# Optimization experiments

Hardware: AMD Instinct MI355X
Metric: run time of the kernel (lower is better)

## Reference

```python
import jax, jax.numpy as jnp
import numpy as np

HIDDEN = 2048
NUM_Q_HEADS = 32
NUM_KV_HEADS = 8
HEAD_DIM = HIDDEN // NUM_Q_HEADS          # 64
GROUP = NUM_Q_HEADS // NUM_KV_HEADS       # 4
B, L = 2, 2048


def setup_inputs() -> dict:
    key = jax.random.key(0)
    ks = jax.random.split(key, 10)
    s = 1.0 / np.sqrt(HIDDEN)
    return {
        "x": jax.random.normal(ks[0], (B, L, HIDDEN), dtype=jnp.float32),
        "attention_mask": jnp.ones((B, L), dtype=jnp.int32),
        "q_w": jax.random.uniform(ks[1], (NUM_Q_HEADS * HEAD_DIM, HIDDEN), jnp.float32, -s, s),
        "q_b": jax.random.uniform(ks[2], (NUM_Q_HEADS * HEAD_DIM,), jnp.float32, -s, s),
        "k_w": jax.random.uniform(ks[3], (NUM_KV_HEADS * HEAD_DIM, HIDDEN), jnp.float32, -s, s),
        "k_b": jax.random.uniform(ks[4], (NUM_KV_HEADS * HEAD_DIM,), jnp.float32, -s, s),
        "v_w": jax.random.uniform(ks[5], (NUM_KV_HEADS * HEAD_DIM, HIDDEN), jnp.float32, -s, s),
        "v_b": jax.random.uniform(ks[6], (NUM_KV_HEADS * HEAD_DIM,), jnp.float32, -s, s),
        "o_w": jax.random.uniform(ks[7], (HIDDEN, HIDDEN), jnp.float32, -s, s),
        "o_b": jax.random.uniform(ks[8], (HIDDEN,), jnp.float32, -s, s),
    }


def reference(x, attention_mask, q_w, q_b, k_w, k_b, v_w, v_b, o_w, o_b):
    Bsz, Ls, _ = x.shape
    # projections (torch Linear: x @ W^T + b)
    q = x @ q_w.T + q_b                      # [B, L, Hq*D]
    k = x @ k_w.T + k_b                      # [B, L, Hkv*D]
    v = x @ v_w.T + v_b                      # [B, L, Hkv*D]
    # grouped reshape: q head h = kv*GROUP + g, matching repeat_interleave on k/v
    q = q.reshape(Bsz, Ls, NUM_KV_HEADS, GROUP, HEAD_DIM)
    k = k.reshape(Bsz, Ls, NUM_KV_HEADS, HEAD_DIM)
    v = v.reshape(Bsz, Ls, NUM_KV_HEADS, HEAD_DIM)
    scale = 1.0 / np.sqrt(HEAD_DIM).astype(np.float32)
    # scores: [B, Hkv, G, Lq, Lk]
    scores = jnp.einsum('bqhgd,bkhd->bhgqk', q, k) * scale
    neg = jnp.finfo(scores.dtype).min
    # causal mask
    causal = jnp.triu(jnp.ones((Ls, Ls), dtype=bool), k=1)
    scores = jnp.where(causal, neg, scores)
    # key padding mask: attention_mask==0 -> masked
    pad = (attention_mask == 0)[:, None, None, None, :]  # [B,1,1,1,Lk]
    scores = jnp.where(pad, neg, scores)
    attn = jax.nn.softmax(scores, axis=-1)
    # dropout is identity in eval / p=0
    out = jnp.einsum('bhgqk,bkhd->bqhgd', attn, v)
    out = out.reshape(Bsz, Ls, HIDDEN)
    return out @ o_w.T + o_b
```

## Files before the change

kernel.cpp:

```cpp
#include <hip/hip_runtime.h>
#include <hip/hip_bf16.h>

typedef __attribute__((ext_vector_type(8))) short s16x8;
typedef __attribute__((ext_vector_type(4))) short s16x4;
typedef __attribute__((ext_vector_type(2))) short s16x2;
typedef __attribute__((ext_vector_type(4))) float f32x4;
typedef __attribute__((ext_vector_type(4))) unsigned int u32x4;

#define L_ 2048
#define HID 2048
#define DH 64

__device__ __forceinline__ short f2bs(float f) {
    __hip_bfloat16 h = __float2bfloat16(f);
    return *reinterpret_cast<short*>(&h);
}
__device__ __forceinline__ unsigned int pkbf_fast(float a, float b) {
    unsigned ua = __builtin_bit_cast(unsigned, a) + 0x8000u;
    unsigned ub = __builtin_bit_cast(unsigned, b) + 0x8000u;
    return __builtin_amdgcn_perm(ub, ua, 0x07060302u);
}
__device__ __forceinline__ float bpermf(int byteidx, float v) {
    int r = __builtin_amdgcn_ds_bpermute(byteidx, __builtin_bit_cast(int, v));
    return __builtin_bit_cast(float, r);
}
__device__ __forceinline__ s16x4 load4_bf16(const float* p) {
    const float4 v = *(const float4*)p;
    s16x4 r; r.x = f2bs(v.x); r.y = f2bs(v.y); r.z = f2bs(v.z); r.w = f2bs(v.w);
    return r;
}
__device__ __forceinline__ s16x4 load4_bf16(const __hip_bfloat16* p) {
    return *(const s16x4*)p;
}
__device__ __forceinline__ void store1(float* p, float v) { *p = v; }
__device__ __forceinline__ void store1(__hip_bfloat16* p, float v) { *p = __float2bfloat16(v); }

__device__ __forceinline__ void glds16(const __hip_bfloat16* g, __hip_bfloat16* l) {
    __builtin_amdgcn_global_load_lds(
        (const __attribute__((address_space(1))) unsigned int*)g,
        (__attribute__((address_space(3))) unsigned int*)l, 16, 0, 0);
}

__device__ __forceinline__ void cvt8_body(const float* src, __hip_bfloat16* dst, long i) {
    const float4* p = (const float4*)src + i * 2;
    const float4 a = p[0], b = p[1];
    s16x8 r;
    r[0] = f2bs(a.x); r[1] = f2bs(a.y); r[2] = f2bs(a.z); r[3] = f2bs(a.w);
    r[4] = f2bs(b.x); r[5] = f2bs(b.y); r[6] = f2bs(b.z); r[7] = f2bs(b.w);
    *((s16x8*)dst + i) = r;
}

__global__ __launch_bounds__(256) void cvt_xqkv(
    const float* __restrict__ x,  const float* __restrict__ qw,
    const float* __restrict__ kw, const float* __restrict__ vw,
    __hip_bfloat16* __restrict__ xb,  __hip_bfloat16* __restrict__ qwb,
    __hip_bfloat16* __restrict__ kwb, __hip_bfloat16* __restrict__ vwb)
{
    long i = (long)blockIdx.x * 256 + threadIdx.x;
    const float* src; __hip_bfloat16* dst;
    if (i < 1048576)      { src = x;  dst = xb;  }
    else if (i < 1572864) { src = qw; dst = qwb; i -= 1048576; }
    else if (i < 1703936) { src = kw; dst = kwb; i -= 1572864; }
    else                  { src = vw; dst = vwb; i -= 1703936; }
    cvt8_body(src, dst, i);
}

__global__ __launch_bounds__(256) void cvt8(const float* __restrict__ in,
                                            __hip_bfloat16* __restrict__ out, int n8) {
    const int i = blockIdx.x * 256 + threadIdx.x;
    if (i >= n8) return;
    cvt8_body(in, out, i);
}

__global__ __launch_bounds__(256) void gemm_qkv(
    const __hip_bfloat16* __restrict__ A,
    const __hip_bfloat16* __restrict__ W,
    const float* __restrict__ qb, const float* __restrict__ kb2,
    const float* __restrict__ vb2,
    __hip_bfloat16* __restrict__ Qb, __hip_bfloat16* __restrict__ Kt,
    __hip_bfloat16* __restrict__ Vt)
{
    const int K = 2048;
    __shared__ __hip_bfloat16 sA[128*32];
    __shared__ __hip_bfloat16 sB[128*32];
    const int tid  = threadIdx.x;
    const int wid  = tid >> 6;
    const int lane = tid & 63;
    const int m0 = blockIdx.x * 128;
    const int n0 = blockIdx.y * 128;
    const int wm = (wid >> 1) * 64;
    const int wn = (wid & 1) * 64;

    f32x4 acc[4][4];
#pragma unroll
    for (int i = 0; i < 4; ++i)
#pragma unroll
        for (int j = 0; j < 4; ++j)
#pragma unroll
            for (int r = 0; r < 4; ++r) acc[i][j][r] = 0.0f;

    const int sr = tid >> 2;
    const int sc = (tid & 3) * 8;
    const __hip_bfloat16* gA = A + (long)(m0 + sr) * K + sc;
    const __hip_bfloat16* gB = W + (long)(n0 + sr) * K + sc;
    __hip_bfloat16* lA = &sA[sr*32 + sc];
    __hip_bfloat16* lB = &sB[sr*32 + sc];

    const int arow0 = wm + (lane & 15);
    const int brow0 = wn + (lane & 15);
    const int koff  = (lane >> 4) * 8;

    for (int kt = 0; kt < 64; ++kt) {
        glds16(gA,              lA);
        glds16(gA + (long)64*K, lA + 64*32);
        glds16(gB,              lB);
        glds16(gB + (long)64*K, lB + 64*32);
        gA += 32; gB += 32;
        __syncthreads();

        s16x8 af[4], bfr[4];
#pragma unroll
        for (int mi = 0; mi < 4; ++mi)
            af[mi] = *(const s16x8*)&sA[(arow0 + mi*16)*32 + koff];
#pragma unroll
        for (int ni = 0; ni < 4; ++ni)
            bfr[ni] = *(const s16x8*)&sB[(brow0 + ni*16)*32 + koff];
#pragma unroll
        for (int mi = 0; mi < 4; ++mi)
#pragma unroll
            for (int ni = 0; ni < 4; ++ni)
                acc[mi][ni] = __builtin_amdgcn_mfma_f32_16x16x32_bf16(
                    af[mi], bfr[ni], acc[mi][ni], 0, 0, 0);
        __syncthreads();
    }

    __hip_bfloat16* C; int ldc, coff; const float* bias;
    if (n0 < 2048)      { C = Qb; ldc = 2048; coff = n0;        bias = qb  + n0; }
    else if (n0 < 2560) { C = Kt; ldc = 512;  coff = n0 - 2048; bias = kb2 + (n0 - 2048); }
    else                { C = Vt; ldc = 512;  coff = n0 - 2560; bias = vb2 + (n0 - 2560); }

    float bvals[4];
#pragma unroll
    for (int ni = 0; ni < 4; ++ni)
        bvals[ni] = bias[wn + ni*16 + (lane & 15)];
#pragma unroll
    for (int mi = 0; mi < 4; ++mi) {
        const int row = m0 + wm + mi*16 + (lane >> 4)*4;
#pragma unroll
        for (int ni = 0; ni < 4; ++ni) {
            const int col = coff + wn + ni*16 + (lane & 15);
#pragma unroll
            for (int r = 0; r < 4; ++r)
                C[(long)(row + r)*ldc + col] = __float2bfloat16(acc[mi][ni][r] + bvals[ni]);
        }
    }
}

template <typename TC>
__global__ __launch_bounds__(256) void gemm_fast(
    const __hip_bfloat16* __restrict__ A,
    const __hip_bfloat16* __restrict__ Bw,
    const float* __restrict__ bias,
    TC* __restrict__ C, int M, int N, int K)
{
    __shared__ __hip_bfloat16 sA[128*32];
    __shared__ __hip_bfloat16 sB[128*32];
    const int tid  = threadIdx.x;
    const int wid  = tid >> 6;
    const int lane = tid & 63;
    const int m0 = blockIdx.x * 128;
    const int n0 = blockIdx.y * 128;
    const int wm = (wid >> 1) * 64;
    const int wn = (wid & 1) * 64;

    f32x4 acc[4][4];
#pragma unroll
    for (int i = 0; i < 4; ++i)
#pragma unroll
        for (int j = 0; j < 4; ++j)
#pragma unroll
            for (int r = 0; r < 4; ++r) acc[i][j][r] = 0.0f;

    const int sr = tid >> 2;
    const int sc = (tid & 3) * 8;
    const __hip_bfloat16* gA = A  + (long)(m0 + sr) * K + sc;
    const __hip_bfloat16* gB = Bw + (long)(n0 + sr) * K + sc;
    __hip_bfloat16* lA = &sA[sr*32 + sc];
    __hip_bfloat16* lB = &sB[sr*32 + sc];

    const int arow0 = wm + (lane & 15);
    const int brow0 = wn + (lane & 15);
    const int koff  = (lane >> 4) * 8;

    const int nk = K >> 5;
    for (int kt = 0; kt < nk; ++kt) {
        glds16(gA,              lA);
        glds16(gA + (long)64*K, lA + 64*32);
        glds16(gB,              lB);
        glds16(gB + (long)64*K, lB + 64*32);
        gA += 32; gB += 32;
        __syncthreads();

        s16x8 af[4], bfr[4];
#pragma unroll
        for (int mi = 0; mi < 4; ++mi)
            af[mi] = *(const s16x8*)&sA[(arow0 + mi*16)*32 + koff];
#pragma unroll
        for (int ni = 0; ni < 4; ++ni)
            bfr[ni] = *(const s16x8*)&sB[(brow0 + ni*16)*32 + koff];
#pragma unroll
        for (int mi = 0; mi < 4; ++mi)
#pragma unroll
            for (int ni = 0; ni < 4; ++ni)
                acc[mi][ni] = __builtin_amdgcn_mfma_f32_16x16x32_bf16(
                    af[mi], bfr[ni], acc[mi][ni], 0, 0, 0);
        __syncthreads();
    }

    float bvals[4];
#pragma unroll
    for (int ni = 0; ni < 4; ++ni)
        bvals[ni] = bias[n0 + wn + ni*16 + (lane & 15)];
#pragma unroll
    for (int mi = 0; mi < 4; ++mi) {
        const int row = m0 + wm + mi*16 + (lane >> 4)*4;
#pragma unroll
        for (int ni = 0; ni < 4; ++ni) {
            const int col = n0 + wn + ni*16 + (lane & 15);
#pragma unroll
            for (int r = 0; r < 4; ++r)
                store1(&C[(long)(row + r)*N + col], acc[mi][ni][r] + bvals[ni]);
        }
    }
}

template <typename TA, typename TC>
__global__ __launch_bounds__(256) void gemm_bt_bias(
    const TA* __restrict__ A, const float* __restrict__ Bw,
    const float* __restrict__ bias, TC* __restrict__ C,
    int M, int N, int K)
{
    __shared__ __hip_bfloat16 sA[128*32];
    __shared__ __hip_bfloat16 sB[128*32];
    const int tid  = threadIdx.x;
    const int wid  = tid >> 6;
    const int lane = tid & 63;
    const int m0 = blockIdx.x * 128;
    const int n0 = blockIdx.y * 128;
    const int wm = (wid >> 1) * 64;
    const int wn = (wid & 1) * 64;

    f32x4 acc[4][4];
#pragma unroll
    for (int i = 0; i < 4; ++i)
#pragma unroll
        for (int j = 0; j < 4; ++j)
#pragma unroll
            for (int r = 0; r < 4; ++r) acc[i][j][r] = 0.0f;

    const int sr = tid >> 3;
    const int sc = (tid & 7) * 4;
    const TA*    gA = A  + (long)(m0 + sr) * K + sc;
    const float* gB = Bw + (long)(n0 + sr) * K + sc;

    const int arow0 = wm + (lane & 15);
    const int brow0 = wn + (lane & 15);
    const int koff  = (lane >> 4) * 8;

    const int nk = K >> 5;
    for (int kt = 0; kt < nk; ++kt) {
        s16x4 a0 = load4_bf16(gA);
        s16x4 a1 = load4_bf16(gA + (long)32*K);
        s16x4 a2 = load4_bf16(gA + (long)64*K);
        s16x4 a3 = load4_bf16(gA + (long)96*K);
        s16x4 b0 = load4_bf16(gB);
        s16x4 b1 = load4_bf16(gB + (long)32*K);
        s16x4 b2 = load4_bf16(gB + (long)64*K);
        s16x4 b3 = load4_bf16(gB + (long)96*K);
        gA += 32; gB += 32;
        *(s16x4*)&sA[(sr     )*32 + sc] = a0;
        *(s16x4*)&sA[(sr + 32)*32 + sc] = a1;
        *(s16x4*)&sA[(sr + 64)*32 + sc] = a2;
        *(s16x4*)&sA[(sr + 96)*32 + sc] = a3;
        *(s16x4*)&sB[(sr     )*32 + sc] = b0;
        *(s16x4*)&sB[(sr + 32)*32 + sc] = b1;
        *(s16x4*)&sB[(sr + 64)*32 + sc] = b2;
        *(s16x4*)&sB[(sr + 96)*32 + sc] = b3;
        __syncthreads();

        s16x8 af[4], bfr[4];
#pragma unroll
        for (int mi = 0; mi < 4; ++mi)
            af[mi] = *(const s16x8*)&sA[(arow0 + mi*16)*32 + koff];
#pragma unroll
        for (int ni = 0; ni < 4; ++ni)
            bfr[ni] = *(const s16x8*)&sB[(brow0 + ni*16)*32 + koff];
#pragma unroll
        for (int mi = 0; mi < 4; ++mi)
#pragma unroll
            for (int ni = 0; ni < 4; ++ni)
                acc[mi][ni] = __builtin_amdgcn_mfma_f32_16x16x32_bf16(
                    af[mi], bfr[ni], acc[mi][ni], 0, 0, 0);
        __syncthreads();
    }

    float bvals[4];
#pragma unroll
    for (int ni = 0; ni < 4; ++ni)
        bvals[ni] = bias[n0 + wn + ni*16 + (lane & 15)];
#pragma unroll
    for (int mi = 0; mi < 4; ++mi) {
        const int row = m0 + wm + mi*16 + (lane >> 4)*4;
#pragma unroll
        for (int ni = 0; ni < 4; ++ni) {
            const int col = n0 + wn + ni*16 + (lane & 15);
#pragma unroll
            for (int r = 0; r < 4; ++r)
                store1(&C[(long)(row + r)*N + col], acc[mi][ni][r] + bvals[ni]);
        }
    }
}

#define LDK 72
#define LDV 72

__global__ __launch_bounds__(512, 6) void gqa_flash(
    const __hip_bfloat16* __restrict__ Q,
    const __hip_bfloat16* __restrict__ Kb,
    const __hip_bfloat16* __restrict__ Vb,
    const int* __restrict__ amask,
    __hip_bfloat16* __restrict__ O)
{
    __shared__ __hip_bfloat16 sK[2][64*LDK];
    __shared__ __hip_bfloat16 sVt[2][64*LDV];
    __shared__ unsigned int sPp[8][512];

    const int tid  = threadIdx.x;
    const int wid  = tid >> 6;
    const int lane = tid & 63;
    const int bx = blockIdx.x;
    const int bh = blockIdx.y;
    const int b  = bh >> 5;
    const int h  = bh & 31;
    const int kv = h >> 2;

    const __hip_bfloat16* Kg = Kb + (long)(b*L_)*512 + kv*DH;
    const __hip_bfloat16* Vg = Vb + (long)(b*L_)*512 + kv*DH;
    const int* mg = amask + b*L_;

    const int lcol = lane & 15;
    const int g    = lane >> 4;

    const int kr = tid >> 3;
    const int kc = (tid & 7) * 8;
    const int vj = (tid & 31) * 2;
    const int vd = (tid >> 5) * 4;
    const int qsr = tid >> 2;
    const int qsc = (tid & 3) * 16;

    unsigned int* myP = sPp[wid];
    const float c1 = 0.18033688011112042f;

    for (int ph = 0; ph < 2; ++ph) {
        const int qt = ph ? (15 - bx) : bx;
        const int jmax = 2*qt + 1;
        const __hip_bfloat16* Qg = Q + (long)(b*L_ + qt*128)*HID + h*DH;

        __syncthreads();
        {
            s16x8 q0 = *(const s16x8*)(Qg + (long)qsr*HID + qsc);
            s16x8 q1 = *(const s16x8*)(Qg + (long)qsr*HID + qsc + 8);
            __hip_bfloat16* dst = (qsr < 64) ? &sK[0][qsr*LDK + qsc]
                                             : &sK[1][(qsr-64)*LDK + qsc];
            *(s16x8*)&dst[0] = q0;
            *(s16x8*)&dst[8] = q1;
        }
        __syncthreads();
        s16x8 qf[2];
        {
            const __hip_bfloat16* qbuf = (wid < 4)
                ? &sK[0][((wid & 3)*16 + lcol)*LDK]
                : &sK[1][((wid & 3)*16 + lcol)*LDK];
            qf[0] = *(const s16x8*)&qbuf[g*8];
            qf[1] = *(const s16x8*)&qbuf[32 + g*8];
        }
        __syncthreads();

        {
            s16x8 k0 = *(const s16x8*)(Kg + (long)kr*512 + kc);
            *(s16x8*)&sK[0][kr*LDK + kc] = k0;
            s16x4 v0 = *(const s16x4*)(Vg + (long)vj*512 + vd);
            s16x4 v1 = *(const s16x4*)(Vg + (long)(vj+1)*512 + vd);
            short* sv = (short*)sVt[0];
#pragma unroll
            for (int i = 0; i < 4; ++i) {
                s16x2 pr; pr.x = v0[i]; pr.y = v1[i];
                *(s16x2*)&sv[(vd+i)*LDV + vj] = pr;
            }
        }

        float lrl = 0.0f;
        f32x4 oacc[4];
#pragma unroll
        for (int nt = 0; nt < 4; ++nt)
#pragma unroll
            for (int r = 0; r < 4; ++r) oacc[nt][r] = 0.0f;

        for (int jt = 0; jt <= jmax; ++jt) {
            const int cur = jt & 1;
            __syncthreads();

            const long pno = (long)((jt + 1)*64) * 512;
            s16x8 kreg = *(const s16x8*)(Kg + pno + (long)kr*512 + kc);
            s16x4 v0r  = *(const s16x4*)(Vg + pno + (long)vj*512 + vd);
            s16x4 v1r  = *(const s16x4*)(Vg + pno + (long)(vj+1)*512 + vd);
            const int mv = mg[jt*64 + lane];
            const unsigned long long bal = __ballot(mv == 0);

            f32x4 sacc[4];
#pragma unroll
            for (int ct = 0; ct < 4; ++ct)
#pragma unroll
                for (int r = 0; r < 4; ++r) sacc[ct][r] = 0.0f;
#pragma unroll
            for (int ks = 0; ks < 2; ++ks)
#pragma unroll
                for (int ct = 0; ct < 4; ++ct) {
                    s16x8 kf = *(const s16x8*)&sK[cur][(ct*16 + lcol)*LDK + ks*32 + g*8];
                    sacc[ct] = __builtin_amdgcn_mfma_f32_16x16x32_bf16(
                        kf, qf[ks], sacc[ct], 0, 0, 0);
                }

            if (bal) {
#pragma unroll
                for (int ct = 0; ct < 4; ++ct) {
                    const unsigned nib = (unsigned)(bal >> (ct*16 + g*4)) & 15u;
#pragma unroll
                    for (int r = 0; r < 4; ++r)
                        if (nib & (1u << r)) sacc[ct][r] = -2.0e5f;
                }
            }
            if (jt >= 2*qt) {
                const int qrow = qt*128 + wid*16 + lcol;
#pragma unroll
                for (int ct = 0; ct < 4; ++ct) {
                    const int jb = jt*64 + ct*16 + g*4;
#pragma unroll
                    for (int r = 0; r < 4; ++r)
                        if (jb + r > qrow) sacc[ct][r] = -2.0e5f;
                }
            }

            float ps = 0.0f;
#pragma unroll
            for (int ct = 0; ct < 4; ++ct) {
                const float p0 = exp2f(sacc[ct][0] * c1);
                const float p1 = exp2f(sacc[ct][1] * c1);
                const float p2 = exp2f(sacc[ct][2] * c1);
                const float p3 = exp2f(sacc[ct][3] * c1);
                ps += (p0 + p1) + (p2 + p3);
                const int xb = (ct & 1) << 4;
                myP[ct*128 +      ((g*16 + lcol) ^ xb)] = pkbf_fast(p0, p1);
                myP[ct*128 + 64 + ((g*16 + lcol) ^ xb)] = pkbf_fast(p2, p3);
            }
            lrl += ps;

            if (jt < jmax) {
                const int nb = cur ^ 1;
                *(s16x8*)&sK[nb][kr*LDK + kc] = kreg;
                short* sv = (short*)sVt[nb];
#pragma unroll
                for (int i = 0; i < 4; ++i) {
                    s16x2 pr; pr.x = v0r[i]; pr.y = v1r[i];
                    *(s16x2*)&sv[(vd+i)*LDV + vj] = pr;
                }
            }

#pragma unroll
            for (int ks = 0; ks < 2; ++ks) {
                const int ct = ks*2 + (g >> 1);
                const int xb = (ct & 1) << 4;
                const int w0 = (2*g) & 3;
                const int w1 = (2*g + 1) & 3;
                u32x4 pu;
                pu.x = myP[ct*128 +      ((w0*16 + lcol) ^ xb)];
                pu.y = myP[ct*128 + 64 + ((w0*16 + lcol) ^ xb)];
                pu.z = myP[ct*128 +      ((w1*16 + lcol) ^ xb)];
                pu.w = myP[ct*128 + 64 + ((w1*16 + lcol) ^ xb)];
                const s16x8 pf = __builtin_bit_cast(s16x8, pu);
#pragma unroll
                for (int nt = 0; nt < 4; ++nt) {
                    s16x8 vf = *(const s16x8*)&sVt[cur][(nt*16 + lcol)*LDV + ks*32 + g*8];
                    oacc[nt] = __builtin_amdgcn_mfma_f32_16x16x32_bf16(
                        pf, vf, oacc[nt], 0, 0, 0);
                }
            }
        }

        lrl += __shfl_xor(lrl, 16);
        lrl += __shfl_xor(lrl, 32);
        const float inv = 1.0f / lrl;
        float invr[4];
#pragma unroll
        for (int r = 0; r < 4; ++r)
            invr[r] = bpermf((g*4 + r) << 2, inv);

        __hip_bfloat16* Og = O + (long)(b*L_ + qt*128)*HID + h*DH;
#pragma unroll
        for (int r = 0; r < 4; ++r) {
            const int row = wid*16 + g*4 + r;
#pragma unroll
            for (int nt = 0; nt < 4; ++nt)
                Og[(long)row*HID + nt*16 + lcol] =
                    __float2bfloat16(oacc[nt][r] * invr[r]);
        }
    }
}

extern "C" void kernel_launch(void* const* d_in, const int* in_sizes, int n_in,
                              void* d_out, int out_size, void* d_ws, size_t ws_size,
                              hipStream_t stream) {
    const float* x   = (const float*)d_in[0];
    const int*   am  = (const int*)d_in[1];
    const float* q_w = (const float*)d_in[2];
    const float* q_b = (const float*)d_in[3];
    const float* k_w = (const float*)d_in[4];
    const float* k_b = (const float*)d_in[5];
    const float* v_w = (const float*)d_in[6];
    const float* v_b = (const float*)d_in[7];
    const float* o_w = (const float*)d_in[8];
    const float* o_b = (const float*)d_in[9];
    float* out = (float*)d_out;
    char* ws = (char*)d_ws;
    dim3 blk(256);

    if (ws_size >= 37748736) {
        __hip_bfloat16* Qb   = (__hip_bfloat16*)d_out;
        __hip_bfloat16* xb   = (__hip_bfloat16*)((char*)d_out + 16777216);
        __hip_bfloat16* wcat = (__hip_bfloat16*)(ws);
        __hip_bfloat16* qwb  = (__hip_bfloat16*)(ws);
        __hip_bfloat16* kwb  = (__hip_bfloat16*)(ws + 8388608);
        __hip_bfloat16* vwb  = (__hip_bfloat16*)(ws + 10485760);
        __hip_bfloat16* Kt   = (__hip_bfloat16*)(ws + 12582912);
        __hip_bfloat16* Vt   = (__hip_bfloat16*)(ws + 16777216);
        __hip_bfloat16* Ob   = (__hip_bfloat16*)(ws + 20971520);
        __hip_bfloat16* owb  = qwb;

        cvt_xqkv<<<7168, blk, 0, stream>>>(x, q_w, k_w, v_w, xb, qwb, kwb, vwb);
        gemm_qkv<<<dim3(32, 24), blk, 0, stream>>>(xb, wcat, q_b, k_b, v_b, Qb, Kt, Vt);
        cvt8<<<2048, blk, 0, stream>>>(o_w, owb, 524288);
        gqa_flash<<<dim3(8, 64), dim3(512), 0, stream>>>(Qb, Kt, Vt, am, Ob);
        gemm_fast<float><<<dim3(32, 16), blk, 0, stream>>>(Ob, owb, o_b, out, 4096, 2048, 2048);
    } else {
        __hip_bfloat16* Qb = (__hip_bfloat16*)d_out;
        __hip_bfloat16* Kt = (__hip_bfloat16*)(ws);
        __hip_bfloat16* Vt = (__hip_bfloat16*)(ws + 4194304);
        __hip_bfloat16* Ob = (__hip_bfloat16*)(ws + 8388608);
        gemm_bt_bias<float, __hip_bfloat16><<<dim3(32,16), blk, 0, stream>>>(x, q_w, q_b, Qb, 4096, 2048, 2048);
        gemm_bt_bias<float, __hip_bfloat16><<<dim3(32, 4), blk, 0, stream>>>(x, k_w, k_b, Kt, 4096,  512, 2048);
        gemm_bt_bias<float, __hip_bfloat16><<<dim3(32, 4), blk, 0, stream>>>(x, v_w, v_b, Vt, 4096,  512, 2048);
        gqa_flash<<<dim3(8, 64), dim3(512), 0, stream>>>(Qb, Kt, Vt, am, Ob);
        gemm_bt_bias<__hip_bfloat16, float><<<dim3(32,16), blk, 0, stream>>>(Ob, o_w, o_b, out, 4096, 2048, 2048);
    }
}
```

Before: 309.5 us.

## Fold softmax scale into Q projection and split paired q-tiles into separate blocks

The log2e/sqrt(d) softmax scale is applied in the QKV GEMM epilogue, so the attention inner loop no longer multiplies each score before exp2. The flash-attention kernel no longer handles two complementary q-tiles per block. It launches one q-tile per block with a doubled grid, ordered longest tiles first. This trades the built-in load balancing of the pairing for more blocks and better CU occupancy, and adds the Q reload and setup cost per block.

```diff
diff --git a/kernel.cpp b/kernel.cpp
--- a/kernel.cpp
+++ b/kernel.cpp
@@ -135,7 +135,9 @@
     }
 
     __hip_bfloat16* C; int ldc, coff; const float* bias;
-    if (n0 < 2048)      { C = Qb; ldc = 2048; coff = n0;        bias = qb  + n0; }
+    float csc = 1.0f;
+    if (n0 < 2048)      { C = Qb; ldc = 2048; coff = n0;        bias = qb  + n0;
+                          csc = 0.18033688011112042f; }
     else if (n0 < 2560) { C = Kt; ldc = 512;  coff = n0 - 2048; bias = kb2 + (n0 - 2048); }
     else                { C = Vt; ldc = 512;  coff = n0 - 2560; bias = vb2 + (n0 - 2560); }
 
@@ -151,7 +153,8 @@
             const int col = coff + wn + ni*16 + (lane & 15);
 #pragma unroll
             for (int r = 0; r < 4; ++r)
-                C[(long)(row + r)*ldc + col] = __float2bfloat16(acc[mi][ni][r] + bvals[ni]);
+                C[(long)(row + r)*ldc + col] =
+                    __float2bfloat16((acc[mi][ni][r] + bvals[ni]) * csc);
         }
     }
 }
@@ -238,7 +241,7 @@
 __global__ __launch_bounds__(256) void gemm_bt_bias(
     const TA* __restrict__ A, const float* __restrict__ Bw,
     const float* __restrict__ bias, TC* __restrict__ C,
-    int M, int N, int K)
+    int M, int N, int K, float scale)
 {
     __shared__ __hip_bfloat16 sA[128*32];
     __shared__ __hip_bfloat16 sB[128*32];
@@ -316,7 +319,8 @@
             const int col = n0 + wn + ni*16 + (lane & 15);
 #pragma unroll
             for (int r = 0; r < 4; ++r)
-                store1(&C[(long)(row + r)*N + col], acc[mi][ni][r] + bvals[ni]);
+                store1(&C[(long)(row + r)*N + col],
+                       (acc[mi][ni][r] + bvals[ni]) * scale);
         }
     }
 }
@@ -338,7 +342,7 @@
     const int tid  = threadIdx.x;
     const int wid  = tid >> 6;
     const int lane = tid & 63;
-    const int bx = blockIdx.x;
+    const int qt = 15 - blockIdx.x;
     const int bh = blockIdx.y;
     const int b  = bh >> 5;
     const int h  = bh & 31;
@@ -359,161 +363,156 @@
     const int qsc = (tid & 3) * 16;
 
     unsigned int* myP = sPp[wid];
-    const float c1 = 0.18033688011112042f;
-
-    for (int ph = 0; ph < 2; ++ph) {
-        const int qt = ph ? (15 - bx) : bx;
-        const int jmax = 2*qt + 1;
-        const __hip_bfloat16* Qg = Q + (long)(b*L_ + qt*128)*HID + h*DH;
-
-        __syncthreads();
-        {
-            s16x8 q0 = *(const s16x8*)(Qg + (long)qsr*HID + qsc);
-            s16x8 q1 = *(const s16x8*)(Qg + (long)qsr*HID + qsc + 8);
-            __hip_bfloat16* dst = (qsr < 64) ? &sK[0][qsr*LDK + qsc]
-                                             : &sK[1][(qsr-64)*LDK + qsc];
-            *(s16x8*)&dst[0] = q0;
-            *(s16x8*)&dst[8] = q1;
-        }
-        __syncthreads();
-        s16x8 qf[2];
-        {
-            const __hip_bfloat16* qbuf = (wid < 4)
-                ? &sK[0][((wid & 3)*16 + lcol)*LDK]
-                : &sK[1][((wid & 3)*16 + lcol)*LDK];
-            qf[0] = *(const s16x8*)&qbuf[g*8];
-            qf[1] = *(const s16x8*)&qbuf[32 + g*8];
-        }
-        __syncthreads();
-
-        {
-            s16x8 k0 = *(const s16x8*)(Kg + (long)kr*512 + kc);
-            *(s16x8*)&sK[0][kr*LDK + kc] = k0;
-            s16x4 v0 = *(const s16x4*)(Vg + (long)vj*512 + vd);
-            s16x4 v1 = *(const s16x4*)(Vg + (long)(vj+1)*512 + vd);
-            short* sv = (short*)sVt[0];
+
+    const int jmax = 2*qt + 1;
+    const __hip_bfloat16* Qg = Q + (long)(b*L_ + qt*128)*HID + h*DH;
+
+    {
+        s16x8 q0 = *(const s16x8*)(Qg + (long)qsr*HID + qsc);
+        s16x8 q1 = *(const s16x8*)(Qg + (long)qsr*HID + qsc + 8);
+        __hip_bfloat16* dst = (qsr < 64) ? &sK[0][qsr*LDK + qsc]
+                                         : &sK[1][(qsr-64)*LDK + qsc];
+        *(s16x8*)&dst[0] = q0;
+        *(s16x8*)&dst[8] = q1;
+    }
+    __syncthreads();
+    s16x8 qf[2];
+    {
+        const __hip_bfloat16* qbuf = (wid < 4)
+            ? &sK[0][((wid & 3)*16 + lcol)*LDK]
+            : &sK[1][((wid & 3)*16 + lcol)*LDK];
+        qf[0] = *(const s16x8*)&qbuf[g*8];
+        qf[1] = *(const s16x8*)&qbuf[32 + g*8];
+    }
+    __syncthreads();
+
+    {
+        s16x8 k0 = *(const s16x8*)(Kg + (long)kr*512 + kc);
+        *(s16x8*)&sK[0][kr*LDK + kc] = k0;
+        s16x4 v0 = *(const s16x4*)(Vg + (long)vj*512 + vd);
+        s16x4 v1 = *(const s16x4*)(Vg + (long)(vj+1)*512 + vd);
+        short* sv = (short*)sVt[0];
+#pragma unroll
+        for (int i = 0; i < 4; ++i) {
+            s16x2 pr; pr.x = v0[i]; pr.y = v1[i];
+            *(s16x2*)&sv[(vd+i)*LDV + vj] = pr;
+        }
+    }
+
+    float lrl = 0.0f;
+    f32x4 oacc[4];
+#pragma unroll
+    for (int nt = 0; nt < 4; ++nt)
+#pragma unroll
+        for (int r = 0; r < 4; ++r) oacc[nt][r] = 0.0f;
+
+    for (int jt = 0; jt <= jmax; ++jt) {
+        const int cur = jt & 1;
+        __syncthreads();
+
+        const long pno = (long)((jt + 1)*64) * 512;
+        s16x8 kreg = *(const s16x8*)(Kg + pno + (long)kr*512 + kc);
+        s16x4 v0r  = *(const s16x4*)(Vg + pno + (long)vj*512 + vd);
+        s16x4 v1r  = *(const s16x4*)(Vg + pno + (long)(vj+1)*512 + vd);
+        const int mv = mg[jt*64 + lane];
+        const unsigned long long bal = __ballot(mv == 0);
+
+        f32x4 sacc[4];
+#pragma unroll
+        for (int ct = 0; ct < 4; ++ct)
+#pragma unroll
+            for (int r = 0; r < 4; ++r) sacc[ct][r] = 0.0f;
+#pragma unroll
+        for (int ks = 0; ks < 2; ++ks)
+#pragma unroll
+            for (int ct = 0; ct < 4; ++ct) {
+                s16x8 kf = *(const s16x8*)&sK[cur][(ct*16 + lcol)*LDK + ks*32 + g*8];
+                sacc[ct] = __builtin_amdgcn_mfma_f32_16x16x32_bf16(
+                    kf, qf[ks], sacc[ct], 0, 0, 0);
+            }
+
+        if (bal) {
+#pragma unroll
+            for (int ct = 0; ct < 4; ++ct) {
+                const unsigned nib = (unsigned)(bal >> (ct*16 + g*4)) & 15u;
+#pragma unroll
+                for (int r = 0; r < 4; ++r)
+                    if (nib & (1u << r)) sacc[ct][r] = -2.0e5f;
+            }
+        }
+        if (jt >= 2*qt) {
+            const int qrow = qt*128 + wid*16 + lcol;
+#pragma unroll
+            for (int ct = 0; ct < 4; ++ct) {
+                const int jb = jt*64 + ct*16 + g*4;
+#pragma unroll
+                for (int r = 0; r < 4; ++r)
+                    if (jb + r > qrow) sacc[ct][r] = -2.0e5f;
+            }
+        }
+
+        float ps = 0.0f;
+#pragma unroll
+        for (int ct = 0; ct < 4; ++ct) {
+            const float p0 = exp2f(sacc[ct][0]);
+            const float p1 = exp2f(sacc[ct][1]);
+            const float p2 = exp2f(sacc[ct][2]);
+            const float p3 = exp2f(sacc[ct][3]);
+            ps += (p0 + p1) + (p2 + p3);
+            const int xb = (ct & 1) << 4;
+            myP[ct*128 +      ((g*16 + lcol) ^ xb)] = pkbf_fast(p0, p1);
+            myP[ct*128 + 64 + ((g*16 + lcol) ^ xb)] = pkbf_fast(p2, p3);
+        }
+        lrl += ps;
+
+        if (jt < jmax) {
+            const int nb = cur ^ 1;
+            *(s16x8*)&sK[nb][kr*LDK + kc] = kreg;
+            short* sv = (short*)sVt[nb];
 #pragma unroll
             for (int i = 0; i < 4; ++i) {
-                s16x2 pr; pr.x = v0[i]; pr.y = v1[i];
+                s16x2 pr; pr.x = v0r[i]; pr.y = v1r[i];
                 *(s16x2*)&sv[(vd+i)*LDV + vj] = pr;
             }
         }
 
-        float lrl = 0.0f;
-        f32x4 oacc[4];
+#pragma unroll
+        for (int ks = 0; ks < 2; ++ks) {
+            const int ct = ks*2 + (g >> 1);
+            const int xb = (ct & 1) << 4;
+            const int w0 = (2*g) & 3;
+            const int w1 = (2*g + 1) & 3;
+            u32x4 pu;
+            pu.x = myP[ct*128 +      ((w0*16 + lcol) ^ xb)];
+            pu.y = myP[ct*128 + 64 + ((w0*16 + lcol) ^ xb)];
+            pu.z = myP[ct*128 +      ((w1*16 + lcol) ^ xb)];
+            pu.w = myP[ct*128 + 64 + ((w1*16 + lcol) ^ xb)];
+            const s16x8 pf = __builtin_bit_cast(s16x8, pu);
+#pragma unroll
+            for (int nt = 0; nt < 4; ++nt) {
+                s16x8 vf = *(const s16x8*)&sVt[cur][(nt*16 + lcol)*LDV + ks*32 + g*8];
+                oacc[nt] = __builtin_amdgcn_mfma_f32_16x16x32_bf16(
+                    pf, vf, oacc[nt], 0, 0, 0);
+            }
+        }
+    }
+
+    lrl += __shfl_xor(lrl, 16);
+    lrl += __shfl_xor(lrl, 32);
+    const float inv = 1.0f / lrl;
+    float invr[4];
+#pragma unroll
+    for (int r = 0; r < 4; ++r)
+        invr[r] = bpermf((g*4 + r) << 2, inv);
+
+    __hip_bfloat16* Og = O + (long)(b*L_ + qt*128)*HID + h*DH;
+#pragma unroll
+    for (int r = 0; r < 4; ++r) {
+        const int row = wid*16 + g*4 + r;
 #pragma unroll
         for (int nt = 0; nt < 4; ++nt)
-#pragma unroll
-            for (int r = 0; r < 4; ++r) oacc[nt][r] = 0.0f;
-
-        for (int jt = 0; jt <= jmax; ++jt) {
-            const int cur = jt & 1;
-            __syncthreads();
-
-            const long pno = (long)((jt + 1)*64) * 512;
-            s16x8 kreg = *(const s16x8*)(Kg + pno + (long)kr*512 + kc);
-            s16x4 v0r  = *(const s16x4*)(Vg + pno + (long)vj*512 + vd);
-            s16x4 v1r  = *(const s16x4*)(Vg + pno + (long)(vj+1)*512 + vd);
-            const int mv = mg[jt*64 + lane];
-            const unsigned long long bal = __ballot(mv == 0);
-
-            f32x4 sacc[4];
-#pragma unroll
-            for (int ct = 0; ct < 4; ++ct)
-#pragma unroll
-                for (int r = 0; r < 4; ++r) sacc[ct][r] = 0.0f;
-#pragma unroll
-            for (int ks = 0; ks < 2; ++ks)
-#pragma unroll
-                for (int ct = 0; ct < 4; ++ct) {
-                    s16x8 kf = *(const s16x8*)&sK[cur][(ct*16 + lcol)*LDK + ks*32 + g*8];
-                    sacc[ct] = __builtin_amdgcn_mfma_f32_16x16x32_bf16(
-                        kf, qf[ks], sacc[ct], 0, 0, 0);
-                }
-
-            if (bal) {
-#pragma unroll
-                for (int ct = 0; ct < 4; ++ct) {
-                    const unsigned nib = (unsigned)(bal >> (ct*16 + g*4)) & 15u;
-#pragma unroll
-                    for (int r = 0; r < 4; ++r)
-                        if (nib & (1u << r)) sacc[ct][r] = -2.0e5f;
-                }
-            }
-            if (jt >= 2*qt) {
-                const int qrow = qt*128 + wid*16 + lcol;
-#pragma unroll
-                for (int ct = 0; ct < 4; ++ct) {
-                    const int jb = jt*64 + ct*16 + g*4;
-#pragma unroll
-                    for (int r = 0; r < 4; ++r)
-                        if (jb + r > qrow) sacc[ct][r] = -2.0e5f;
-                }
-            }
-
-            float ps = 0.0f;
-#pragma unroll
-            for (int ct = 0; ct < 4; ++ct) {
-                const float p0 = exp2f(sacc[ct][0] * c1);
-                const float p1 = exp2f(sacc[ct][1] * c1);
-                const float p2 = exp2f(sacc[ct][2] * c1);
-                const float p3 = exp2f(sacc[ct][3] * c1);
-                ps += (p0 + p1) + (p2 + p3);
-                const int xb = (ct & 1) << 4;
-                myP[ct*128 +      ((g*16 + lcol) ^ xb)] = pkbf_fast(p0, p1);
-                myP[ct*128 + 64 + ((g*16 + lcol) ^ xb)] = pkbf_fast(p2, p3);
-            }
-            lrl += ps;
-
-            if (jt < jmax) {
-                const int nb = cur ^ 1;
-                *(s16x8*)&sK[nb][kr*LDK + kc] = kreg;
-                short* sv = (short*)sVt[nb];
-#pragma unroll
-                for (int i = 0; i < 4; ++i) {
-                    s16x2 pr; pr.x = v0r[i]; pr.y = v1r[i];
-                    *(s16x2*)&sv[(vd+i)*LDV + vj] = pr;
-                }
-            }
-
-#pragma unroll
-            for (int ks = 0; ks < 2; ++ks) {
-                const int ct = ks*2 + (g >> 1);
-                const int xb = (ct & 1) << 4;
-                const int w0 = (2*g) & 3;
-                const int w1 = (2*g + 1) & 3;
-                u32x4 pu;
-                pu.x = myP[ct*128 +      ((w0*16 + lcol) ^ xb)];
-                pu.y = myP[ct*128 + 64 + ((w0*16 + lcol) ^ xb)];
-                pu.z = myP[ct*128 +      ((w1*16 + lcol) ^ xb)];
-                pu.w = myP[ct*128 + 64 + ((w1*16 + lcol) ^ xb)];
-                const s16x8 pf = __builtin_bit_cast(s16x8, pu);
-#pragma unroll
-                for (int nt = 0; nt < 4; ++nt) {
-                    s16x8 vf = *(const s16x8*)&sVt[cur][(nt*16 + lcol)*LDV + ks*32 + g*8];
-                    oacc[nt] = __builtin_amdgcn_mfma_f32_16x16x32_bf16(
-                        pf, vf, oacc[nt], 0, 0, 0);
-                }
-            }
-        }
-
-        lrl += __shfl_xor(lrl, 16);
-        lrl += __shfl_xor(lrl, 32);
-        const float inv = 1.0f / lrl;
-        float invr[4];
-#pragma unroll
-        for (int r = 0; r < 4; ++r)
-            invr[r] = bpermf((g*4 + r) << 2, inv);
-
-        __hip_bfloat16* Og = O + (long)(b*L_ + qt*128)*HID + h*DH;
-#pragma unroll
-        for (int r = 0; r < 4; ++r) {
-            const int row = wid*16 + g*4 + r;
-#pragma unroll
-            for (int nt = 0; nt < 4; ++nt)
-                Og[(long)row*HID + nt*16 + lcol] =
-                    __float2bfloat16(oacc[nt][r] * invr[r]);
-        }
+            Og[(long)row*HID + nt*16 + lcol] =
+                __float2bfloat16(oacc[nt][r] * invr[r]);
     }
 }
 
@@ -533,6 +532,7 @@
     float* out = (float*)d_out;
     char* ws = (char*)d_ws;
     dim3 blk(256);
+    const float qsc = 0.18033688011112042f;
 
     if (ws_size >= 37748736) {
         __hip_bfloat16* Qb   = (__hip_bfloat16*)d_out;
@@ -549,17 +549,17 @@
         cvt_xqkv<<<7168, blk, 0, stream>>>(x, q_w, k_w, v_w, xb, qwb, kwb, vwb);
         gemm_qkv<<<dim3(32, 24), blk, 0, stream>>>(xb, wcat, q_b, k_b, v_b, Qb, Kt, Vt);
         cvt8<<<2048, blk, 0, stream>>>(o_w, owb, 524288);
-        gqa_flash<<<dim3(8, 64), dim3(512), 0, stream>>>(Qb, Kt, Vt, am, Ob);
+        gqa_flash<<<dim3(16, 64), dim3(512), 0, stream>>>(Qb, Kt, Vt, am, Ob);
         gemm_fast<float><<<dim3(32, 16), blk, 0, stream>>>(Ob, owb, o_b, out, 4096, 2048, 2048);
     } else {
         __hip_bfloat16* Qb = (__hip_bfloat16*)d_out;
         __hip_bfloat16* Kt = (__hip_bfloat16*)(ws);
         __hip_bfloat16* Vt = (__hip_bfloat16*)(ws + 4194304);
         __hip_bfloat16* Ob = (__hip_bfloat16*)(ws + 8388608);
-        gemm_bt_bias<float, __hip_bfloat16><<<dim3(32,16), blk, 0, stream>>>(x, q_w, q_b, Qb, 4096, 2048, 2048);
-        gemm_bt_bias<float, __hip_bfloat16><<<dim3(32, 4), blk, 0, stream>>>(x, k_w, k_b, Kt, 4096,  512, 2048);
-        gemm_bt_bias<float, __hip_bfloat16><<<dim3(32, 4), blk, 0, stream>>>(x, v_w, v_b, Vt, 4096,  512, 2048);
-        gqa_flash<<<dim3(8, 64), dim3(512), 0, stream>>>(Qb, Kt, Vt, am, Ob);
-        gemm_bt_bias<__hip_bfloat16, float><<<dim3(32,16), blk, 0, stream>>>(Ob, o_w, o_b, out, 4096, 2048, 2048);
-    }
-}
+        gemm_bt_bias<float, __hip_bfloat16><<<dim3(32,16), blk, 0, stream>>>(x, q_w, q_b, Qb, 4096, 2048, 2048, qsc);
+        gemm_bt_bias<float, __hip_bfloat16><<<dim3(32, 4), blk, 0, stream>>>(x, k_w, k_b, Kt, 4096,  512, 2048, 1.0f);
+        gemm_bt_bias<float, __hip_bfloat16><<<dim3(32, 4), blk, 0, stream>>>(x, v_w, v_b, Vt, 4096,  512, 2048, 1.0f);
+        gqa_flash<<<dim3(16, 64), dim3(512), 0, stream>>>(Qb, Kt, Vt, am, Ob);
+        gemm_bt_bias<__hip_bfloat16, float><<<dim3(32,16), blk, 0, stream>>>(Ob, o_w, o_b, out, 4096, 2048, 2048, 1.0f);
+    }
+}
```

Measured after the change: 355.5 us. 1.15x slower.
